# Performance work log

Measured on AMD Instinct MI355X. Metric: run time of the kernel, lower is better.

The kernel has to match this reference:

```python
import jax, jax.numpy as jnp
import numpy as np

# Config matching init_kwargs: num_heads=4, embedding_dim=1024 -> per-head dim 256,
# num_embeddings=8192. Defaults: hierarchical=False, transitions=False, gumbel=False,
# learnable_priors=False, relative_error=False, ema=True (so no q_latent_loss),
# use_straight_through=True, code_offset=0. Eval-mode path: hard argmin code selection.
H = 4
K = 8192
D = 1024
d = D // H
B = 8192
COMMITMENT_COST = 0.25
INIT_SCALE = 0.5


def setup_inputs() -> dict:
    key = jax.random.key(0)
    k1, k2 = jax.random.split(key)
    inputs = jax.random.normal(k1, (B, 1, D), dtype=jnp.float32)
    # embedding.weight.data.normal_(std=init_scale * init_decay_weight**hix), decay_weight=1.0
    codebooks = jax.random.normal(k2, (H, K, d), dtype=jnp.float32) * INIT_SCALE
    return {"inputs": inputs, "codebooks": codebooks}


def reference(inputs, codebooks):
    # inputs: [B, 1, D]; codebooks: [H, K, d]
    b = inputs.shape[0]
    x = inputs[:, 0, :].reshape(b, H, d)  # per-head slices of the latent

    x2 = jnp.sum(x * x, axis=-1)                       # [B, H]
    e2 = jnp.sum(codebooks * codebooks, axis=-1)       # [H, K]
    xe = jnp.einsum('bhd,hkd->bhk', x, codebooks)      # [B, H, K]
    dist = x2[..., None] - 2.0 * xe + e2[None, :, :]

    # Hard code selection (eval path: argmin over codebook)
    codes = jnp.argmin(dist, axis=-1)                  # [B, H] int

    # Gather quantized vectors: q[b, h] = codebooks[h, codes[b, h]]
    q = codebooks[jnp.arange(H)[None, :], codes]       # [B, H, d]

    # Commitment loss per sample (EMA mode => no codebook loss term):
    # F.mse_loss(quantized.detach(), this_input, reduction='none').mean(dim=-1), summed over heads
    e_latent = jnp.mean((jax.lax.stop_gradient(q) - x) ** 2, axis=-1)  # [B, H]
    loss = COMMITMENT_COST * jnp.sum(e_latent, axis=-1)                 # [B]

    # Straight-through estimator
    q_st = x + jax.lax.stop_gradient(q - x)            # [B, H, d]
    quantized = q_st.reshape(b, 1, D)

    return loss, quantized, codes
```

## Files before the change

kernel.cpp:

```cpp
#include <hip/hip_runtime.h>
#include <math.h>

#define HH 4
#define KK 8192
#define DD 1024
#define HD 256
#define BB 8192
#define MARGINF 1.0625f

typedef __attribute__((ext_vector_type(8))) short short8;
typedef __attribute__((ext_vector_type(4))) float floatx4;

__device__ __forceinline__ unsigned short f2bf(float f) {
    unsigned int u = __float_as_uint(f);
    u += 0x7FFFu + ((u >> 16) & 1u);
    return (unsigned short)(u >> 16);
}

__device__ __forceinline__ void gl_lds16(const unsigned short* g, char* l) {
    __builtin_amdgcn_global_load_lds(
        (const __attribute__((address_space(1))) unsigned int*)g,
        (__attribute__((address_space(3))) unsigned int*)l, 16, 0, 0);
}

__device__ __forceinline__ void gl_lds4(const float* g, char* l) {
    __builtin_amdgcn_global_load_lds(
        (const __attribute__((address_space(1))) unsigned int*)g,
        (__attribute__((address_space(3))) unsigned int*)l, 4, 0, 0);
}

__global__ __launch_bounds__(256)
void vq_e2(const float* __restrict__ C, float* __restrict__ e2w, float* __restrict__ e2p) {
    int gid  = blockIdx.x * 256 + threadIdx.x;
    int code = gid >> 2;
    int part = gid & 3;
    const float4* p = (const float4*)&C[(size_t)code * HD + part * 64];
    float s = 0.f;
#pragma unroll
    for (int i = 0; i < 16; ++i) {
        float4 v = p[i];
        s = fmaf(v.x, v.x, s); s = fmaf(v.y, v.y, s);
        s = fmaf(v.z, v.z, s); s = fmaf(v.w, v.w, s);
    }
    s += __shfl_xor(s, 1);
    s += __shfl_xor(s, 2);
    if (part == 0) { e2w[code] = s; e2p[code] = s + 1024.0f; }
}

__global__ __launch_bounds__(256)
void vq_cvtC(const float* __restrict__ C, unsigned short* __restrict__ Cbf) {
    size_t i = ((size_t)blockIdx.x * 256 + threadIdx.x) * 8;
    float4 a = *(const float4*)&C[i];
    float4 b = *(const float4*)&C[i + 4];
    short8 o;
    o[0] = (short)f2bf(a.x); o[1] = (short)f2bf(a.y); o[2] = (short)f2bf(a.z); o[3] = (short)f2bf(a.w);
    o[4] = (short)f2bf(b.x); o[5] = (short)f2bf(b.y); o[6] = (short)f2bf(b.z); o[7] = (short)f2bf(b.w);
    *(short8*)&Cbf[i] = o;
}

#define WAITV(N) asm volatile("s_waitcnt vmcnt(" #N ")" ::: "memory")
#define VQ_SYNC() do { __builtin_amdgcn_s_barrier(); __builtin_amdgcn_sched_barrier(0); } while (0)

#define VQ_STAGE(SB)                                                                                   \
    do {                                                                                               \
        const int ch1_ = (SB) >> 2, ks1_ = (SB) & 3;                                                   \
        _Pragma("unroll")                                                                              \
        for (int j = 0; j < 4; ++j) {                                                                  \
            const unsigned short* gp_ = CbfH + (size_t)(ch1_ * 128 + j * 32 + c0) * HD + ks1_ * 64 + ksegS * 8; \
            gl_lds16(gp_, smB + (((SB) & 3) << 14) + ((j * 256 + wid * 64) << 4));                     \
        }                                                                                              \
    } while (0)

#define VQ_STAGE_E2(CH2)                                                                               \
    do {                                                                                               \
        const int chc_ = (CH2) > 63 ? 63 : (CH2);                                                      \
        const float* gp_ = e2p + (size_t)h * KK + chc_ * 128 + ((wid & 1) << 6) + lane;                \
        gl_lds4(gp_, (char*)&e2ring[(((CH2) & 3) << 7) + ((wid & 1) << 6)]);                           \
    } while (0)

#define VQ_COMPUTE(KST, CH, S)                                                                         \
    do {                                                                                               \
        if ((KST) == 0) {                                                                              \
            e0 = e2ring[(((CH) & 3) << 7) + wid * 32 + cl];                                            \
            e1 = e2ring[(((CH) & 3) << 7) + wid * 32 + 16 + cl];                                       \
            floatx4 zz = {0.f, 0.f, 0.f, 0.f};                                                         \
            _Pragma("unroll")                                                                          \
            for (int tm = 0; tm < 4; ++tm) { acc[tm][0] = zz; acc[tm][1] = zz; }                       \
        }                                                                                              \
        const char* bb_ = smB + (((S) & 3) << 14);                                                     \
        __builtin_amdgcn_s_setprio(1);                                                                 \
        _Pragma("unroll")                                                                              \
        for (int kc = 0; kc < 2; ++kc) {                                                               \
            short8 b0 = *(const short8*)(bb_ + roff[0][kc]);                                           \
            short8 b1 = *(const short8*)(bb_ + roff[1][kc]);                                           \
            const int ai = (KST) * 2 + kc;                                                             \
            _Pragma("unroll")                                                                          \
            for (int tm = 0; tm < 4; ++tm) {                                                           \
                acc[tm][0] = __builtin_amdgcn_mfma_f32_16x16x32_bf16(afrag[tm][ai], b0, acc[tm][0], 0, 0, 0); \
                acc[tm][1] = __builtin_amdgcn_mfma_f32_16x16x32_bf16(afrag[tm][ai], b1, acc[tm][1], 0, 0, 0); \
            }                                                                                          \
        }                                                                                              \
        __builtin_amdgcn_s_setprio(0);                                                                 \
        if ((KST) == 3) {                                                                              \
            const int ctag = (CH) << 1;                                                                \
            _Pragma("unroll")                                                                          \
            for (int tn = 0; tn < 2; ++tn) {                                                           \
                const float ee = tn ? e1 : e0;                                                         \
                const int tag = ctag | tn;                                                             \
                _Pragma("unroll")                                                                      \
                for (int tm = 0; tm < 4; ++tm)                                                         \
                    _Pragma("unroll")                                                                  \
                    for (int r = 0; r < 4; ++r) {                                                      \
                        float dp = fmaf(-2.0f, acc[tm][tn][r], ee);                                    \
                        int key = (__float_as_int(dp) & 0xFFFFFF80) | tag;                             \
                        const int sl = tm * 4 + r;                                                     \
                        int mx = max(key, best1[sl]);                                                  \
                        best1[sl] = min(best1[sl], key);                                               \
                        best2[sl] = min(best2[sl], mx);                                                \
                    }                                                                                  \
            }                                                                                          \
        }                                                                                              \
    } while (0)

__global__ __launch_bounds__(256, 2)
void vq_score(const float* __restrict__ X, const float* __restrict__ C,
              const unsigned short* __restrict__ Cbf,
              const float* __restrict__ e2w, const float* __restrict__ e2p,
              float* __restrict__ elw,
              float* __restrict__ out_q, float* __restrict__ out_codes) {
    __shared__ __align__(16) char smB[65536];
    __shared__ float e2ring[512];
    __shared__ int   rowWave[256];
    __shared__ int   rowMinS[64];
    __shared__ int   cntA[64];
    __shared__ int   listI[64 * 8];
    __shared__ float pairD[128];
    __shared__ int   pairI[128];
    __shared__ int   codeS[64];

    const int tid = threadIdx.x;
    const int bi  = blockIdx.x;
    const int x   = bi & 7;
    const int h   = x & 3;
    const int rowbase = (((bi >> 3) << 1) + (x >> 2)) * 64;
    const int wid  = tid >> 6;
    const int lane = tid & 63;
    const int cl = lane & 15;
    const int qh = lane >> 4;

    short8 afrag[4][8];
#pragma unroll
    for (int tm = 0; tm < 4; ++tm) {
        const float* rp = X + (size_t)(rowbase + tm * 16 + cl) * DD + h * HD + qh * 8;
#pragma unroll
        for (int i = 0; i < 8; ++i) {
            float4 v0 = *(const float4*)(rp + i * 32);
            float4 v1 = *(const float4*)(rp + i * 32 + 4);
            short8 t;
            t[0] = (short)f2bf(v0.x); t[1] = (short)f2bf(v0.y); t[2] = (short)f2bf(v0.z); t[3] = (short)f2bf(v0.w);
            t[4] = (short)f2bf(v1.x); t[5] = (short)f2bf(v1.y); t[6] = (short)f2bf(v1.z); t[7] = (short)f2bf(v1.w);
            afrag[tm][i] = t;
        }
    }

    int best1[16], best2[16];
#pragma unroll
    for (int i = 0; i < 16; ++i) { best1[i] = 0x7FFFFFFF; best2[i] = 0x7FFFFFFF; }

    const unsigned short* CbfH = Cbf + (size_t)h * KK * HD;
    const int c0    = tid >> 3;
    const int ksegS = (tid & 7) ^ (c0 & 7);
    int roff[2][2];
#pragma unroll
    for (int tn = 0; tn < 2; ++tn)
#pragma unroll
        for (int kc = 0; kc < 2; ++kc)
            roff[tn][kc] = (wid * 32 + tn * 16 + cl) * 128 + ((((kc << 2) + qh) ^ (cl & 7)) << 4);

    floatx4 acc[4][2];
    float e0 = 0.f, e1 = 0.f;

    VQ_STAGE_E2(0);
    VQ_STAGE_E2(1);
    VQ_STAGE(0);
    VQ_STAGE(1);
    VQ_STAGE(2);

    for (int ch = 0; ch < 63; ++ch) {
        const int s0 = ch << 2;
        WAITV(8); VQ_SYNC(); VQ_STAGE(s0 + 3); VQ_STAGE_E2(ch + 2); VQ_COMPUTE(0, ch, s0 + 0);
        WAITV(9); VQ_SYNC(); VQ_STAGE(s0 + 4);                      VQ_COMPUTE(1, ch, s0 + 1);
        WAITV(9); VQ_SYNC(); VQ_STAGE(s0 + 5);                      VQ_COMPUTE(2, ch, s0 + 2);
        WAITV(9); VQ_SYNC(); VQ_STAGE(s0 + 6);                      VQ_COMPUTE(3, ch, s0 + 3);
    }
    WAITV(8); VQ_SYNC(); VQ_STAGE(255); VQ_COMPUTE(0, 63, 252);
    WAITV(8); VQ_SYNC();                VQ_COMPUTE(1, 63, 253);
    WAITV(4); VQ_SYNC();                VQ_COMPUTE(2, 63, 254);
    WAITV(0); VQ_SYNC();                VQ_COMPUTE(3, 63, 255);

#pragma unroll
    for (int sl = 0; sl < 16; ++sl) {
        int m = best1[sl];
        m = min(m, __shfl_xor(m, 1));
        m = min(m, __shfl_xor(m, 2));
        m = min(m, __shfl_xor(m, 4));
        m = min(m, __shfl_xor(m, 8));
        if (cl == 0) {
            int row = (sl >> 2) * 16 + qh * 4 + (sl & 3);
            rowWave[wid * 64 + row] = m;
        }
    }
    __syncthreads();
    if (tid < 64) {
        rowMinS[tid] = min(min(rowWave[tid], rowWave[64 + tid]),
                           min(rowWave[128 + tid], rowWave[192 + tid]));
        cntA[tid] = 0;
    }
    __syncthreads();
#pragma unroll
    for (int sl = 0; sl < 16; ++sl) {
        const int row = (sl >> 2) * 16 + qh * 4 + (sl & 3);
        const float lim = __int_as_float(rowMinS[row]) + MARGINF;
#pragma unroll
        for (int t = 0; t < 2; ++t) {
            int key = t ? best2[sl] : best1[sl];
            float d = __int_as_float(key & 0xFFFFFF80);
            if (d <= lim) {
                int chunk = (key >> 1) & 63, tn = key & 1;
                int code = chunk * 128 + wid * 32 + tn * 16 + cl;
                int pos = atomicAdd(&cntA[row], 1);
                if (pos < 8) listI[row * 8 + pos] = code;
            }
        }
    }
    __syncthreads();
    if (tid < 128) {
        int row = tid >> 1, par = tid & 1;
        int n = min(cntA[row], 8);
        float bD = 1e38f; int bI = 0x7FFFFFFF;
        if (n == 1) {
            if (par == 0) { bD = -1e38f; bI = listI[row * 8]; }
        } else {
            const float* Xr = X + (size_t)(rowbase + row) * DD + h * HD;
            float p0 = 0, p1 = 0, p2 = 0, p3 = 0;
            for (int d = 0;   d < 64;  ++d) p0 = fmaf(Xr[d], Xr[d], p0);
            for (int d = 64;  d < 128; ++d) p1 = fmaf(Xr[d], Xr[d], p1);
            for (int d = 128; d < 192; ++d) p2 = fmaf(Xr[d], Xr[d], p2);
            for (int d = 192; d < 256; ++d) p3 = fmaf(Xr[d], Xr[d], p3);
            float x2 = __fadd_rn(__fadd_rn(p0, p1), __fadd_rn(p2, p3));
            for (int j = par; j < n; j += 2) {
                int idx = listI[row * 8 + j];
                const float* Cr = C + ((size_t)h * KK + idx) * HD;
                float a = 0.f;
                for (int d = 0; d < 256; ++d) a = fmaf(Xr[d], Cr[d], a);
                float t1 = fmaf(-2.0f, a, x2);
                float dist = __fadd_rn(t1, e2w[h * KK + idx]);
                if (dist < bD || (dist == bD && idx < bI)) { bD = dist; bI = idx; }
            }
        }
        pairD[tid] = bD; pairI[tid] = bI;
    }
    __syncthreads();
    if (tid < 64) {
        float d0 = pairD[tid * 2], d1 = pairD[tid * 2 + 1];
        int   i0 = pairI[tid * 2], i1 = pairI[tid * 2 + 1];
        int w = (d1 < d0 || (d1 == d0 && i1 < i0)) ? i1 : i0;
        codeS[tid] = w;
        out_codes[(size_t)(rowbase + tid) * HH + h] = (float)w;
    }
    __syncthreads();

    {
        int row = tid >> 2, part = tid & 3;
        int b = rowbase + row;
        int c = codeS[row];
        const float4* qp = (const float4*)&C[((size_t)h * KK + c) * HD + part * 64];
        const float4* xp = (const float4*)&X[(size_t)b * DD + h * HD + part * 64];
        float4*       op = (float4*)&out_q[(size_t)b * DD + h * HD + part * 64];
        float s = 0.f;
#pragma unroll
        for (int i = 0; i < 16; ++i) {
            float4 q4 = qp[i]; float4 x4 = xp[i]; float4 o;
            float d0 = __fsub_rn(q4.x, x4.x); o.x = __fadd_rn(x4.x, d0); s = fmaf(d0, d0, s);
            float d1 = __fsub_rn(q4.y, x4.y); o.y = __fadd_rn(x4.y, d1); s = fmaf(d1, d1, s);
            float d2 = __fsub_rn(q4.z, x4.z); o.z = __fadd_rn(x4.z, d2); s = fmaf(d2, d2, s);
            float d3 = __fsub_rn(q4.w, x4.w); o.w = __fadd_rn(x4.w, d3); s = fmaf(d3, d3, s);
            op[i] = o;
        }
        s += __shfl_xor(s, 1);
        s += __shfl_xor(s, 2);
        if (part == 0) elw[(size_t)b * HH + h] = s * (1.0f / 256.0f);
    }
}

__global__ __launch_bounds__(256)
void vq_loss(const float* __restrict__ elw, float* __restrict__ out_loss) {
    int b = blockIdx.x * 256 + threadIdx.x;
    if (b < BB) {
        float4 e = *(const float4*)&elw[(size_t)b * HH];
        out_loss[b] = 0.25f * (((e.x + e.y) + e.z) + e.w);
    }
}

#define ROWS 64
#define KC   128
#define DC   32

__global__ __launch_bounds__(256, 3)
void vq_main(const float* __restrict__ X, const float* __restrict__ C,
             const float* __restrict__ e2w, float* __restrict__ elw,
             float* __restrict__ out_q, float* __restrict__ out_codes) {
    __shared__ float smem[2048 + 4096];
    float* Xs = smem;
    float* Cs = smem + 2048;
    __shared__ float x2s[ROWS];
    __shared__ int   codeSf[ROWS];

    const int tid     = threadIdx.x;
    const int h       = blockIdx.y;
    const int rowbase = blockIdx.x * ROWS;

    {
        int row = tid >> 2, part = tid & 3;
        const float4* xp = (const float4*)&X[(size_t)(rowbase + row) * DD + h * HD + part * 64];
        float s = 0.f;
#pragma unroll
        for (int i = 0; i < 16; ++i) {
            float4 v = xp[i];
            s = fmaf(v.x, v.x, s); s = fmaf(v.y, v.y, s);
            s = fmaf(v.z, v.z, s); s = fmaf(v.w, v.w, s);
        }
        s += __shfl_xor(s, 1);
        s += __shfl_xor(s, 2);
        if (part == 0) x2s[row] = s;
    }
    __syncthreads();

    const int rg = tid & 7;
    const int cg = tid >> 3;
    const int r0 = rg * 8;

    float x2r[8];
#pragma unroll
    for (int r = 0; r < 8; ++r) x2r[r] = x2s[r0 + r];

    float mn[8]; int mi[8];
#pragma unroll
    for (int r = 0; r < 8; ++r) { mn[r] = 3.402823466e38f; mi[r] = 0; }

    for (int kb = 0; kb < KK; kb += KC) {
        float acc[8][4];
#pragma unroll
        for (int r = 0; r < 8; ++r)
#pragma unroll
            for (int c = 0; c < 4; ++c) acc[r][c] = 0.f;

        for (int db = 0; db < HD; db += DC) {
            __syncthreads();
#pragma unroll
            for (int rep = 0; rep < 2; ++rep) {
                int i = tid + rep * 256;
                int row = i >> 3, q = i & 7;
                float4 v = *(const float4*)&X[(size_t)(rowbase + row) * DD + h * HD + db + q * 4];
                int col = row ^ ((q & 3) << 3);
                Xs[(q * 4 + 0) * 64 + col] = v.x;
                Xs[(q * 4 + 1) * 64 + col] = v.y;
                Xs[(q * 4 + 2) * 64 + col] = v.z;
                Xs[(q * 4 + 3) * 64 + col] = v.w;
            }
#pragma unroll
            for (int rep = 0; rep < 4; ++rep) {
                int i = tid + rep * 256;
                int code = i >> 3, q = i & 7;
                float4 v = *(const float4*)&C[((size_t)(h * KK + kb + code)) * HD + db + q * 4];
                int col = code ^ ((q & 3) << 3);
                Cs[(q * 4 + 0) * 128 + col] = v.x;
                Cs[(q * 4 + 1) * 128 + col] = v.y;
                Cs[(q * 4 + 2) * 128 + col] = v.z;
                Cs[(q * 4 + 3) * 128 + col] = v.w;
            }
            __syncthreads();
#pragma unroll
            for (int t = 0; t < DC; ++t) {
                int sw = ((t >> 2) & 3) << 3;
                const float4 xa = *(const float4*)&Xs[t * 64 + (r0 ^ sw)];
                const float4 xb = *(const float4*)&Xs[t * 64 + ((r0 ^ sw) + 4)];
                const float4 cv = *(const float4*)&Cs[t * 128 + ((cg * 4) ^ sw)];
                float xv[8] = {xa.x, xa.y, xa.z, xa.w, xb.x, xb.y, xb.z, xb.w};
                float clv[4] = {cv.x, cv.y, cv.z, cv.w};
#pragma unroll
                for (int r = 0; r < 8; ++r)
#pragma unroll
                    for (int c = 0; c < 4; ++c)
                        acc[r][c] = fmaf(xv[r], clv[c], acc[r][c]);
            }
        }
        const float4 e2v = *(const float4*)&e2w[h * KK + kb + cg * 4];
        float e2a[4] = {e2v.x, e2v.y, e2v.z, e2v.w};
#pragma unroll
        for (int c = 0; c < 4; ++c) {
            int kidx = kb + cg * 4 + c;
#pragma unroll
            for (int r = 0; r < 8; ++r) {
                float t1   = x2r[r] - 2.0f * acc[r][c];
                float dist = __fadd_rn(t1, e2a[c]);
                if (dist < mn[r]) { mn[r] = dist; mi[r] = kidx; }
            }
        }
    }

    __syncthreads();
    float* redm = smem;
    int*   redi = (int*)(smem + 2048);
#pragma unroll
    for (int r = 0; r < 8; ++r) {
        redm[cg * 64 + r0 + r] = mn[r];
        redi[cg * 64 + r0 + r] = mi[r];
    }
    __syncthreads();
    if (tid < ROWS) {
        int row = tid;
        float best = redm[row]; int bi2 = redi[row];
        for (int gg = 1; gg < 32; ++gg) {
            float m = redm[gg * 64 + row]; int ii = redi[gg * 64 + row];
            if (m < best || (m == best && ii < bi2)) { best = m; bi2 = ii; }
        }
        codeSf[row] = bi2;
        out_codes[(size_t)(rowbase + row) * HH + h] = (float)bi2;
    }
    __syncthreads();

    {
        int row = tid >> 2, part = tid & 3;
        int b = rowbase + row;
        int c = codeSf[row];
        const float4* qp = (const float4*)&C[((size_t)(h * KK + c)) * HD + part * 64];
        const float4* xp = (const float4*)&X[(size_t)b * DD + h * HD + part * 64];
        float4*       op = (float4*)&out_q[(size_t)b * DD + h * HD + part * 64];
        float s = 0.f;
#pragma unroll
        for (int i = 0; i < 16; ++i) {
            float4 q4 = qp[i]; float4 x4 = xp[i]; float4 o;
            float d0 = __fsub_rn(q4.x, x4.x); o.x = __fadd_rn(x4.x, d0); s = fmaf(d0, d0, s);
            float d1 = __fsub_rn(q4.y, x4.y); o.y = __fadd_rn(x4.y, d1); s = fmaf(d1, d1, s);
            float d2 = __fsub_rn(q4.z, x4.z); o.z = __fadd_rn(x4.z, d2); s = fmaf(d2, d2, s);
            float d3 = __fsub_rn(q4.w, x4.w); o.w = __fadd_rn(x4.w, d3); s = fmaf(d3, d3, s);
            op[i] = o;
        }
        s += __shfl_xor(s, 1);
        s += __shfl_xor(s, 2);
        if (part == 0) elw[(size_t)b * HH + h] = s * (1.0f / 256.0f);
    }
}

extern "C" void kernel_launch(void* const* d_in, const int* in_sizes, int n_in,
                              void* d_out, int out_size, void* d_ws, size_t ws_size,
                              hipStream_t stream) {
    const float* X = (const float*)d_in[0];
    const float* C = (const float*)d_in[1];
    float* out      = (float*)d_out;
    float* out_loss = out;
    float* out_q    = out + BB;
    float* out_code = out + BB + (size_t)BB * DD;
    float* e2w = (float*)d_ws;
    float* e2p = e2w + (size_t)HH * KK;
    float* elw = e2p + (size_t)HH * KK;
    unsigned short* Cbf = (unsigned short*)(elw + (size_t)BB * HH);

    const size_t need = ((size_t)2 * HH * KK + (size_t)BB * HH) * 4 + (size_t)HH * KK * HD * 2;

    if (ws_size >= need) {
        vq_e2<<<512, 256, 0, stream>>>(C, e2w, e2p);
        vq_cvtC<<<(HH * KK * HD / 8) / 256, 256, 0, stream>>>(C, Cbf);
        vq_score<<<512, 256, 0, stream>>>(X, C, Cbf, e2w, e2p, elw, out_q, out_code);
        vq_loss<<<BB / 256, 256, 0, stream>>>(elw, out_loss);
    } else {
        vq_e2<<<512, 256, 0, stream>>>(C, e2w, e2p);
        dim3 grid(BB / ROWS, HH);
        vq_main<<<grid, 256, 0, stream>>>(X, C, e2w, elw, out_q, out_code);
        vq_loss<<<BB / 256, 256, 0, stream>>>(elw, out_loss);
    }
}
```

Before: 306.1 us.

## Double score-block rows to 128 with 512 threads and fuse codebook prep kernels

```diff
diff --git a/kernel.cpp b/kernel.cpp
--- a/kernel.cpp
+++ b/kernel.cpp
@@ -27,6 +27,33 @@
     __builtin_amdgcn_global_load_lds(
         (const __attribute__((address_space(1))) unsigned int*)g,
         (__attribute__((address_space(3))) unsigned int*)l, 4, 0, 0);
+}
+
+__global__ __launch_bounds__(256)
+void vq_prep(const float* __restrict__ C, unsigned short* __restrict__ Cbf,
+             float* __restrict__ e2w, float* __restrict__ e2p) {
+    int gid  = blockIdx.x * 256 + threadIdx.x;
+    int code = gid >> 2;
+    int part = gid & 3;
+    const float4* p = (const float4*)&C[(size_t)code * HD + part * 64];
+    short8* ob = (short8*)&Cbf[(size_t)code * HD + part * 64];
+    float s = 0.f;
+#pragma unroll
+    for (int i = 0; i < 8; ++i) {
+        float4 a = p[2 * i];
+        float4 b = p[2 * i + 1];
+        s = fmaf(a.x, a.x, s); s = fmaf(a.y, a.y, s);
+        s = fmaf(a.z, a.z, s); s = fmaf(a.w, a.w, s);
+        s = fmaf(b.x, b.x, s); s = fmaf(b.y, b.y, s);
+        s = fmaf(b.z, b.z, s); s = fmaf(b.w, b.w, s);
+        short8 o;
+        o[0] = (short)f2bf(a.x); o[1] = (short)f2bf(a.y); o[2] = (short)f2bf(a.z); o[3] = (short)f2bf(a.w);
+        o[4] = (short)f2bf(b.x); o[5] = (short)f2bf(b.y); o[6] = (short)f2bf(b.z); o[7] = (short)f2bf(b.w);
+        ob[i] = o;
+    }
+    s += __shfl_xor(s, 1);
+    s += __shfl_xor(s, 2);
+    if (part == 0) { e2w[code] = s; e2p[code] = s + 1024.0f; }
 }
 
 __global__ __launch_bounds__(256)
@@ -47,53 +74,42 @@
     if (part == 0) { e2w[code] = s; e2p[code] = s + 1024.0f; }
 }
 
-__global__ __launch_bounds__(256)
-void vq_cvtC(const float* __restrict__ C, unsigned short* __restrict__ Cbf) {
-    size_t i = ((size_t)blockIdx.x * 256 + threadIdx.x) * 8;
-    float4 a = *(const float4*)&C[i];
-    float4 b = *(const float4*)&C[i + 4];
-    short8 o;
-    o[0] = (short)f2bf(a.x); o[1] = (short)f2bf(a.y); o[2] = (short)f2bf(a.z); o[3] = (short)f2bf(a.w);
-    o[4] = (short)f2bf(b.x); o[5] = (short)f2bf(b.y); o[6] = (short)f2bf(b.z); o[7] = (short)f2bf(b.w);
-    *(short8*)&Cbf[i] = o;
-}
-
 #define WAITV(N) asm volatile("s_waitcnt vmcnt(" #N ")" ::: "memory")
 #define VQ_SYNC() do { __builtin_amdgcn_s_barrier(); __builtin_amdgcn_sched_barrier(0); } while (0)
 
 #define VQ_STAGE(SB)                                                                                   \
     do {                                                                                               \
-        const int ch1_ = (SB) >> 2, ks1_ = (SB) & 3;                                                   \
+        const int ch_ = (SB) >> 1, kh_ = (SB) & 1;                                                     \
         _Pragma("unroll")                                                                              \
         for (int j = 0; j < 4; ++j) {                                                                  \
-            const unsigned short* gp_ = CbfH + (size_t)(ch1_ * 128 + j * 32 + c0) * HD + ks1_ * 64 + ksegS * 8; \
-            gl_lds16(gp_, smB + (((SB) & 3) << 14) + ((j * 256 + wid * 64) << 4));                     \
+            const unsigned short* gp_ = CbfH + (size_t)(ch_ * 128 + j * 32 + (tid >> 4)) * HD          \
+                                        + kh_ * 128 + ksegS * 8;                                       \
+            gl_lds16(gp_, smB + (((SB) & 3) << 15) + ((j * 512 + wid * 64) << 4));                     \
         }                                                                                              \
     } while (0)
 
 #define VQ_STAGE_E2(CH2)                                                                               \
     do {                                                                                               \
-        const int chc_ = (CH2) > 63 ? 63 : (CH2);                                                      \
-        const float* gp_ = e2p + (size_t)h * KK + chc_ * 128 + ((wid & 1) << 6) + lane;                \
+        const float* gp_ = e2p + (size_t)h * KK + (CH2) * 128 + ((wid & 1) << 6) + lane;               \
         gl_lds4(gp_, (char*)&e2ring[(((CH2) & 3) << 7) + ((wid & 1) << 6)]);                           \
     } while (0)
 
 #define VQ_COMPUTE(KST, CH, S)                                                                         \
     do {                                                                                               \
         if ((KST) == 0) {                                                                              \
-            e0 = e2ring[(((CH) & 3) << 7) + wid * 32 + cl];                                            \
-            e1 = e2ring[(((CH) & 3) << 7) + wid * 32 + 16 + cl];                                       \
+            e0 = e2ring[(((CH) & 3) << 7) + wq * 32 + cl];                                             \
+            e1 = e2ring[(((CH) & 3) << 7) + wq * 32 + 16 + cl];                                        \
             floatx4 zz = {0.f, 0.f, 0.f, 0.f};                                                         \
             _Pragma("unroll")                                                                          \
             for (int tm = 0; tm < 4; ++tm) { acc[tm][0] = zz; acc[tm][1] = zz; }                       \
         }                                                                                              \
-        const char* bb_ = smB + (((S) & 3) << 14);                                                     \
+        const char* bb_ = smB + (((S) & 3) << 15);                                                     \
         __builtin_amdgcn_s_setprio(1);                                                                 \
         _Pragma("unroll")                                                                              \
-        for (int kc = 0; kc < 2; ++kc) {                                                               \
-            short8 b0 = *(const short8*)(bb_ + roff[0][kc]);                                           \
-            short8 b1 = *(const short8*)(bb_ + roff[1][kc]);                                           \
-            const int ai = (KST) * 2 + kc;                                                             \
+        for (int ks = 0; ks < 4; ++ks) {                                                               \
+            short8 b0 = *(const short8*)(bb_ + roff[0][ks]);                                           \
+            short8 b1 = *(const short8*)(bb_ + roff[1][ks]);                                           \
+            const int ai = (KST) * 4 + ks;                                                             \
             _Pragma("unroll")                                                                          \
             for (int tm = 0; tm < 4; ++tm) {                                                           \
                 acc[tm][0] = __builtin_amdgcn_mfma_f32_16x16x32_bf16(afrag[tm][ai], b0, acc[tm][0], 0, 0, 0); \
@@ -101,7 +117,7 @@
             }                                                                                          \
         }                                                                                              \
         __builtin_amdgcn_s_setprio(0);                                                                 \
-        if ((KST) == 3) {                                                                              \
+        if ((KST) == 1) {                                                                              \
             const int ctag = (CH) << 1;                                                                \
             _Pragma("unroll")                                                                          \
             for (int tn = 0; tn < 2; ++tn) {                                                           \
@@ -114,44 +130,46 @@
                         float dp = fmaf(-2.0f, acc[tm][tn][r], ee);                                    \
                         int key = (__float_as_int(dp) & 0xFFFFFF80) | tag;                             \
                         const int sl = tm * 4 + r;                                                     \
-                        int mx = max(key, best1[sl]);                                                  \
-                        best1[sl] = min(best1[sl], key);                                               \
-                        best2[sl] = min(best2[sl], mx);                                                \
+                        int b1o = best1[sl];                                                           \
+                        best1[sl] = min(b1o, key);                                                     \
+                        best2[sl] = min(best2[sl], max(key, b1o));                   \
                     }                                                                                  \
             }                                                                                          \
         }                                                                                              \
     } while (0)
 
-__global__ __launch_bounds__(256, 2)
+__global__ __launch_bounds__(512, 2)
 void vq_score(const float* __restrict__ X, const float* __restrict__ C,
               const unsigned short* __restrict__ Cbf,
               const float* __restrict__ e2w, const float* __restrict__ e2p,
               float* __restrict__ elw,
               float* __restrict__ out_q, float* __restrict__ out_codes) {
-    __shared__ __align__(16) char smB[65536];
+    __shared__ __align__(16) char smB[131072];
     __shared__ float e2ring[512];
-    __shared__ int   rowWave[256];
-    __shared__ int   rowMinS[64];
-    __shared__ int   cntA[64];
-    __shared__ int   listI[64 * 8];
-    __shared__ float pairD[128];
-    __shared__ int   pairI[128];
-    __shared__ int   codeS[64];
+    __shared__ int   rowWave[512];
+    __shared__ int   rowMinS[128];
+    __shared__ int   cntA[128];
+    __shared__ int   listI[128 * 8];
+    __shared__ float pairD[256];
+    __shared__ int   pairI[256];
+    __shared__ int   codeS[128];
 
     const int tid = threadIdx.x;
     const int bi  = blockIdx.x;
     const int x   = bi & 7;
     const int h   = x & 3;
-    const int rowbase = (((bi >> 3) << 1) + (x >> 2)) * 64;
+    const int rowbase = (((bi >> 3) << 1) + (x >> 2)) * 128;
     const int wid  = tid >> 6;
     const int lane = tid & 63;
     const int cl = lane & 15;
     const int qh = lane >> 4;
+    const int wq = wid & 3;
+    const int rh = wid >> 2;
 
     short8 afrag[4][8];
 #pragma unroll
     for (int tm = 0; tm < 4; ++tm) {
-        const float* rp = X + (size_t)(rowbase + tm * 16 + cl) * DD + h * HD + qh * 8;
+        const float* rp = X + (size_t)(rowbase + rh * 64 + tm * 16 + cl) * DD + h * HD + qh * 8;
 #pragma unroll
         for (int i = 0; i < 8; ++i) {
             float4 v0 = *(const float4*)(rp + i * 32);
@@ -168,35 +186,34 @@
     for (int i = 0; i < 16; ++i) { best1[i] = 0x7FFFFFFF; best2[i] = 0x7FFFFFFF; }
 
     const unsigned short* CbfH = Cbf + (size_t)h * KK * HD;
-    const int c0    = tid >> 3;
-    const int ksegS = (tid & 7) ^ (c0 & 7);
-    int roff[2][2];
+    const int ksegS = (tid & 15) ^ ((tid >> 4) & 15);
+    int roff[2][4];
 #pragma unroll
     for (int tn = 0; tn < 2; ++tn)
 #pragma unroll
-        for (int kc = 0; kc < 2; ++kc)
-            roff[tn][kc] = (wid * 32 + tn * 16 + cl) * 128 + ((((kc << 2) + qh) ^ (cl & 7)) << 4);
+        for (int ks = 0; ks < 4; ++ks)
+            roff[tn][ks] = (wq * 32 + tn * 16 + cl) * 256 + ((((ks << 2) + qh) ^ cl) << 4);
 
     floatx4 acc[4][2];
     float e0 = 0.f, e1 = 0.f;
 
+    asm volatile("s_waitcnt vmcnt(0)" ::: "memory");
+
     VQ_STAGE_E2(0);
+    VQ_STAGE(0);
     VQ_STAGE_E2(1);
-    VQ_STAGE(0);
     VQ_STAGE(1);
     VQ_STAGE(2);
 
-    for (int ch = 0; ch < 63; ++ch) {
-        const int s0 = ch << 2;
-        WAITV(8); VQ_SYNC(); VQ_STAGE(s0 + 3); VQ_STAGE_E2(ch + 2); VQ_COMPUTE(0, ch, s0 + 0);
+    for (int ch = 0; ch < 62; ++ch) {
+        const int s0 = ch << 1;
+        WAITV(9); VQ_SYNC(); VQ_STAGE(s0 + 3); VQ_STAGE_E2(ch + 2); VQ_COMPUTE(0, ch, s0);
         WAITV(9); VQ_SYNC(); VQ_STAGE(s0 + 4);                      VQ_COMPUTE(1, ch, s0 + 1);
-        WAITV(9); VQ_SYNC(); VQ_STAGE(s0 + 5);                      VQ_COMPUTE(2, ch, s0 + 2);
-        WAITV(9); VQ_SYNC(); VQ_STAGE(s0 + 6);                      VQ_COMPUTE(3, ch, s0 + 3);
-    }
-    WAITV(8); VQ_SYNC(); VQ_STAGE(255); VQ_COMPUTE(0, 63, 252);
-    WAITV(8); VQ_SYNC();                VQ_COMPUTE(1, 63, 253);
-    WAITV(4); VQ_SYNC();                VQ_COMPUTE(2, 63, 254);
-    WAITV(0); VQ_SYNC();                VQ_COMPUTE(3, 63, 255);
+    }
+    WAITV(9); VQ_SYNC(); VQ_STAGE(127); VQ_COMPUTE(0, 62, 124);
+    WAITV(9); VQ_SYNC();                VQ_COMPUTE(1, 62, 125);
+    WAITV(4); VQ_SYNC();                VQ_COMPUTE(0, 63, 126);
+    WAITV(0); VQ_SYNC();                VQ_COMPUTE(1, 63, 127);
 
 #pragma unroll
     for (int sl = 0; sl < 16; ++sl) {
@@ -206,20 +223,20 @@
         m = min(m, __shfl_xor(m, 4));
         m = min(m, __shfl_xor(m, 8));
         if (cl == 0) {
-            int row = (sl >> 2) * 16 + qh * 4 + (sl & 3);
-            rowWave[wid * 64 + row] = m;
-        }
-    }
-    __syncthreads();
-    if (tid < 64) {
-        rowMinS[tid] = min(min(rowWave[tid], rowWave[64 + tid]),
-                           min(rowWave[128 + tid], rowWave[192 + tid]));
+            int row = rh * 64 + (sl >> 2) * 16 + qh * 4 + (sl & 3);
+            rowWave[wq * 128 + row] = m;
+        }
+    }
+    __syncthreads();
+    if (tid < 128) {
+        rowMinS[tid] = min(min(rowWave[tid], rowWave[128 + tid]),
+                           min(rowWave[256 + tid], rowWave[384 + tid]));
         cntA[tid] = 0;
     }
     __syncthreads();
 #pragma unroll
     for (int sl = 0; sl < 16; ++sl) {
-        const int row = (sl >> 2) * 16 + qh * 4 + (sl & 3);
+        const int row = rh * 64 + (sl >> 2) * 16 + qh * 4 + (sl & 3);
         const float lim = __int_as_float(rowMinS[row]) + MARGINF;
 #pragma unroll
         for (int t = 0; t < 2; ++t) {
@@ -227,14 +244,14 @@
             float d = __int_as_float(key & 0xFFFFFF80);
             if (d <= lim) {
                 int chunk = (key >> 1) & 63, tn = key & 1;
-                int code = chunk * 128 + wid * 32 + tn * 16 + cl;
+                int code = chunk * 128 + wq * 32 + tn * 16 + cl;
                 int pos = atomicAdd(&cntA[row], 1);
                 if (pos < 8) listI[row * 8 + pos] = code;
             }
         }
     }
     __syncthreads();
-    if (tid < 128) {
+    if (tid < 256) {
         int row = tid >> 1, par = tid & 1;
         int n = min(cntA[row], 8);
         float bD = 1e38f; int bI = 0x7FFFFFFF;
@@ -261,7 +278,7 @@
         pairD[tid] = bD; pairI[tid] = bI;
     }
     __syncthreads();
-    if (tid < 64) {
+    if (tid < 128) {
         float d0 = pairD[tid * 2], d1 = pairD[tid * 2 + 1];
         int   i0 = pairI[tid * 2], i1 = pairI[tid * 2 + 1];
         int w = (d1 < d0 || (d1 == d0 && i1 < i0)) ? i1 : i0;
@@ -470,9 +487,8 @@
     const size_t need = ((size_t)2 * HH * KK + (size_t)BB * HH) * 4 + (size_t)HH * KK * HD * 2;
 
     if (ws_size >= need) {
-        vq_e2<<<512, 256, 0, stream>>>(C, e2w, e2p);
-        vq_cvtC<<<(HH * KK * HD / 8) / 256, 256, 0, stream>>>(C, Cbf);
-        vq_score<<<512, 256, 0, stream>>>(X, C, Cbf, e2w, e2p, elw, out_q, out_code);
+        vq_prep<<<512, 256, 0, stream>>>(C, Cbf, e2w, e2p);
+        vq_score<<<256, 512, 0, stream>>>(X, C, Cbf, e2w, e2p, elw, out_q, out_code);
         vq_loss<<<BB / 256, 256, 0, stream>>>(elw, out_loss);
     } else {
         vq_e2<<<512, 256, 0, stream>>>(C, e2w, e2p);
```

Measured after the change: 318.8 us. +4.1%, slower.

## Fuse prep kernels, drop block barriers via per-wave staging, fold loss into score

Applied to the files above, without the earlier changes.

```diff
diff --git a/kernel.cpp b/kernel.cpp
--- a/kernel.cpp
+++ b/kernel.cpp
@@ -11,6 +11,8 @@
 typedef __attribute__((ext_vector_type(8))) short short8;
 typedef __attribute__((ext_vector_type(4))) float floatx4;
 
+__device__ unsigned int vq_cnt[128];
+
 __device__ __forceinline__ unsigned short f2bf(float f) {
     unsigned int u = __float_as_uint(f);
     u += 0x7FFFu + ((u >> 16) & 1u);
@@ -27,6 +29,33 @@
     __builtin_amdgcn_global_load_lds(
         (const __attribute__((address_space(1))) unsigned int*)g,
         (__attribute__((address_space(3))) unsigned int*)l, 4, 0, 0);
+}
+
+__global__ __launch_bounds__(256)
+void vq_prep(const float* __restrict__ C, unsigned short* __restrict__ Cbf,
+             float* __restrict__ e2w, float* __restrict__ e2p) {
+    int gid  = blockIdx.x * 256 + threadIdx.x;
+    int code = gid >> 2;
+    int part = gid & 3;
+    const float4* p = (const float4*)&C[(size_t)code * HD + part * 64];
+    short8* ob = (short8*)&Cbf[(size_t)code * HD + part * 64];
+    float s = 0.f;
+#pragma unroll
+    for (int i = 0; i < 8; ++i) {
+        float4 a = p[2 * i];
+        float4 b = p[2 * i + 1];
+        s = fmaf(a.x, a.x, s); s = fmaf(a.y, a.y, s);
+        s = fmaf(a.z, a.z, s); s = fmaf(a.w, a.w, s);
+        s = fmaf(b.x, b.x, s); s = fmaf(b.y, b.y, s);
+        s = fmaf(b.z, b.z, s); s = fmaf(b.w, b.w, s);
+        short8 o;
+        o[0] = (short)f2bf(a.x); o[1] = (short)f2bf(a.y); o[2] = (short)f2bf(a.z); o[3] = (short)f2bf(a.w);
+        o[4] = (short)f2bf(b.x); o[5] = (short)f2bf(b.y); o[6] = (short)f2bf(b.z); o[7] = (short)f2bf(b.w);
+        ob[i] = o;
+    }
+    s += __shfl_xor(s, 1);
+    s += __shfl_xor(s, 2);
+    if (part == 0) { e2w[code] = s; e2p[code] = s + 1024.0f; }
 }
 
 __global__ __launch_bounds__(256)
@@ -47,42 +76,35 @@
     if (part == 0) { e2w[code] = s; e2p[code] = s + 1024.0f; }
 }
 
-__global__ __launch_bounds__(256)
-void vq_cvtC(const float* __restrict__ C, unsigned short* __restrict__ Cbf) {
-    size_t i = ((size_t)blockIdx.x * 256 + threadIdx.x) * 8;
-    float4 a = *(const float4*)&C[i];
-    float4 b = *(const float4*)&C[i + 4];
-    short8 o;
-    o[0] = (short)f2bf(a.x); o[1] = (short)f2bf(a.y); o[2] = (short)f2bf(a.z); o[3] = (short)f2bf(a.w);
-    o[4] = (short)f2bf(b.x); o[5] = (short)f2bf(b.y); o[6] = (short)f2bf(b.z); o[7] = (short)f2bf(b.w);
-    *(short8*)&Cbf[i] = o;
-}
-
-#define WAITV(N) asm volatile("s_waitcnt vmcnt(" #N ")" ::: "memory")
-#define VQ_SYNC() do { __builtin_amdgcn_s_barrier(); __builtin_amdgcn_sched_barrier(0); } while (0)
+#define WAITV(N)                                                                                       \
+    do {                                                                                               \
+        asm volatile("s_waitcnt vmcnt(" #N ")" ::: "memory");                                          \
+        __builtin_amdgcn_sched_barrier(0);                                                             \
+    } while (0)
 
 #define VQ_STAGE(SB)                                                                                   \
     do {                                                                                               \
-        const int ch1_ = (SB) >> 2, ks1_ = (SB) & 3;                                                   \
+        const int ch_ = (SB) >> 2, ks_ = (SB) & 3;                                                     \
         _Pragma("unroll")                                                                              \
         for (int j = 0; j < 4; ++j) {                                                                  \
-            const unsigned short* gp_ = CbfH + (size_t)(ch1_ * 128 + j * 32 + c0) * HD + ks1_ * 64 + ksegS * 8; \
-            gl_lds16(gp_, smB + (((SB) & 3) << 14) + ((j * 256 + wid * 64) << 4));                     \
+            const unsigned short* gp_ = CbfH + (size_t)(ch_ * 128 + wid * 32 + j * 8 + (lane >> 3)) * HD \
+                                        + ks_ * 64 + kseg2 * 8;                                        \
+            gl_lds16(gp_, smB + (((SB) & 3) << 14) + (wid << 12) + (j << 10));                         \
         }                                                                                              \
     } while (0)
 
 #define VQ_STAGE_E2(CH2)                                                                               \
     do {                                                                                               \
         const int chc_ = (CH2) > 63 ? 63 : (CH2);                                                      \
-        const float* gp_ = e2p + (size_t)h * KK + chc_ * 128 + ((wid & 1) << 6) + lane;                \
-        gl_lds4(gp_, (char*)&e2ring[(((CH2) & 3) << 7) + ((wid & 1) << 6)]);                           \
+        const float* gp_ = e2p + (size_t)h * KK + chc_ * 128 + wid * 32 + (lane & 31);                 \
+        gl_lds4(gp_, (char*)e2ring + (wid << 10) + (((CH2) & 3) << 8));                                \
     } while (0)
 
 #define VQ_COMPUTE(KST, CH, S)                                                                         \
     do {                                                                                               \
         if ((KST) == 0) {                                                                              \
-            e0 = e2ring[(((CH) & 3) << 7) + wid * 32 + cl];                                            \
-            e1 = e2ring[(((CH) & 3) << 7) + wid * 32 + 16 + cl];                                       \
+            e0 = e2ring[wid * 256 + (((CH) & 3) << 6) + cl];                                           \
+            e1 = e2ring[wid * 256 + (((CH) & 3) << 6) + 16 + cl];                                      \
             floatx4 zz = {0.f, 0.f, 0.f, 0.f};                                                         \
             _Pragma("unroll")                                                                          \
             for (int tm = 0; tm < 4; ++tm) { acc[tm][0] = zz; acc[tm][1] = zz; }                       \
@@ -114,9 +136,9 @@
                         float dp = fmaf(-2.0f, acc[tm][tn][r], ee);                                    \
                         int key = (__float_as_int(dp) & 0xFFFFFF80) | tag;                             \
                         const int sl = tm * 4 + r;                                                     \
-                        int mx = max(key, best1[sl]);                                                  \
-                        best1[sl] = min(best1[sl], key);                                               \
-                        best2[sl] = min(best2[sl], mx);                                                \
+                        int b1o = best1[sl];                                                           \
+                        best1[sl] = min(b1o, key);                                                     \
+                        best2[sl] = min(best2[sl], max(key, b1o));                                     \
                     }                                                                                  \
             }                                                                                          \
         }                                                                                              \
@@ -127,9 +149,10 @@
               const unsigned short* __restrict__ Cbf,
               const float* __restrict__ e2w, const float* __restrict__ e2p,
               float* __restrict__ elw,
-              float* __restrict__ out_q, float* __restrict__ out_codes) {
+              float* __restrict__ out_q, float* __restrict__ out_codes,
+              float* __restrict__ out_loss) {
     __shared__ __align__(16) char smB[65536];
-    __shared__ float e2ring[512];
+    __shared__ float e2ring[1024];
     __shared__ int   rowWave[256];
     __shared__ int   rowMinS[64];
     __shared__ int   cntA[64];
@@ -137,6 +160,7 @@
     __shared__ float pairD[128];
     __shared__ int   pairI[128];
     __shared__ int   codeS[64];
+    __shared__ int   lastFlag;
 
     const int tid = threadIdx.x;
     const int bi  = blockIdx.x;
@@ -168,8 +192,7 @@
     for (int i = 0; i < 16; ++i) { best1[i] = 0x7FFFFFFF; best2[i] = 0x7FFFFFFF; }
 
     const unsigned short* CbfH = Cbf + (size_t)h * KK * HD;
-    const int c0    = tid >> 3;
-    const int ksegS = (tid & 7) ^ (c0 & 7);
+    const int kseg2 = (lane & 7) ^ ((lane >> 3) & 7);
     int roff[2][2];
 #pragma unroll
     for (int tn = 0; tn < 2; ++tn)
@@ -180,23 +203,25 @@
     floatx4 acc[4][2];
     float e0 = 0.f, e1 = 0.f;
 
+    asm volatile("s_waitcnt vmcnt(0)" ::: "memory");
+
     VQ_STAGE_E2(0);
+    VQ_STAGE(0);
     VQ_STAGE_E2(1);
-    VQ_STAGE(0);
     VQ_STAGE(1);
     VQ_STAGE(2);
 
     for (int ch = 0; ch < 63; ++ch) {
         const int s0 = ch << 2;
-        WAITV(8); VQ_SYNC(); VQ_STAGE(s0 + 3); VQ_STAGE_E2(ch + 2); VQ_COMPUTE(0, ch, s0 + 0);
-        WAITV(9); VQ_SYNC(); VQ_STAGE(s0 + 4);                      VQ_COMPUTE(1, ch, s0 + 1);
-        WAITV(9); VQ_SYNC(); VQ_STAGE(s0 + 5);                      VQ_COMPUTE(2, ch, s0 + 2);
-        WAITV(9); VQ_SYNC(); VQ_STAGE(s0 + 6);                      VQ_COMPUTE(3, ch, s0 + 3);
-    }
-    WAITV(8); VQ_SYNC(); VQ_STAGE(255); VQ_COMPUTE(0, 63, 252);
-    WAITV(8); VQ_SYNC();                VQ_COMPUTE(1, 63, 253);
-    WAITV(4); VQ_SYNC();                VQ_COMPUTE(2, 63, 254);
-    WAITV(0); VQ_SYNC();                VQ_COMPUTE(3, 63, 255);
+        WAITV(8); VQ_STAGE(s0 + 3); VQ_STAGE_E2(ch + 2); VQ_COMPUTE(0, ch, s0);
+        WAITV(9); VQ_STAGE(s0 + 4);                      VQ_COMPUTE(1, ch, s0 + 1);
+        WAITV(9); VQ_STAGE(s0 + 5);                      VQ_COMPUTE(2, ch, s0 + 2);
+        WAITV(9); VQ_STAGE(s0 + 6);                      VQ_COMPUTE(3, ch, s0 + 3);
+    }
+    WAITV(8); VQ_STAGE(255); VQ_COMPUTE(0, 63, 252);
+    WAITV(8);                VQ_COMPUTE(1, 63, 253);
+    WAITV(4);                VQ_COMPUTE(2, 63, 254);
+    WAITV(0);                VQ_COMPUTE(3, 63, 255);
 
 #pragma unroll
     for (int sl = 0; sl < 16; ++sl) {
@@ -289,7 +314,26 @@
         }
         s += __shfl_xor(s, 1);
         s += __shfl_xor(s, 2);
-        if (part == 0) elw[(size_t)b * HH + h] = s * (1.0f / 256.0f);
+        if (part == 0) elw[(size_t)h * BB + b] = s * (1.0f / 256.0f);
+    }
+
+    __threadfence();
+    __syncthreads();
+    if (tid == 0) {
+        unsigned int old = atomicAdd(&vq_cnt[rowbase >> 6], 1u);
+        lastFlag = ((old & 3u) == 3u) ? 1 : 0;
+    }
+    __syncthreads();
+    if (lastFlag) {
+        __threadfence();
+        if (tid < 64) {
+            int b = rowbase + tid;
+            float ev0 = elw[0 * BB + b];
+            float ev1 = elw[1 * BB + b];
+            float ev2 = elw[2 * BB + b];
+            float ev3 = elw[3 * BB + b];
+            out_loss[b] = 0.25f * (((ev0 + ev1) + ev2) + ev3);
+        }
     }
 }
 
@@ -470,10 +514,8 @@
     const size_t need = ((size_t)2 * HH * KK + (size_t)BB * HH) * 4 + (size_t)HH * KK * HD * 2;
 
     if (ws_size >= need) {
-        vq_e2<<<512, 256, 0, stream>>>(C, e2w, e2p);
-        vq_cvtC<<<(HH * KK * HD / 8) / 256, 256, 0, stream>>>(C, Cbf);
-        vq_score<<<512, 256, 0, stream>>>(X, C, Cbf, e2w, e2p, elw, out_q, out_code);
-        vq_loss<<<BB / 256, 256, 0, stream>>>(elw, out_loss);
+        vq_prep<<<512, 256, 0, stream>>>(C, Cbf, e2w, e2p);
+        vq_score<<<512, 256, 0, stream>>>(X, C, Cbf, e2w, e2p, elw, out_q, out_code, out_loss);
     } else {
         vq_e2<<<512, 256, 0, stream>>>(C, e2w, e2p);
         dim3 grid(BB / ROWS, HH);
```

Result: slower. 440.5 us (+43.9%).

## Deepen LDS staging ring to eight stages and fuse codebook prep kernels

Applied to the files above, without the earlier changes.

```diff
diff --git a/kernel.cpp b/kernel.cpp
--- a/kernel.cpp
+++ b/kernel.cpp
@@ -27,6 +27,33 @@
     __builtin_amdgcn_global_load_lds(
         (const __attribute__((address_space(1))) unsigned int*)g,
         (__attribute__((address_space(3))) unsigned int*)l, 4, 0, 0);
+}
+
+__global__ __launch_bounds__(256)
+void vq_prep(const float* __restrict__ C, unsigned short* __restrict__ Cbf,
+             float* __restrict__ e2w, float* __restrict__ e2p) {
+    int gid  = blockIdx.x * 256 + threadIdx.x;
+    int code = gid >> 2;
+    int part = gid & 3;
+    const float4* p = (const float4*)&C[(size_t)code * HD + part * 64];
+    short8* ob = (short8*)&Cbf[(size_t)code * HD + part * 64];
+    float s = 0.f;
+#pragma unroll
+    for (int i = 0; i < 8; ++i) {
+        float4 a = p[2 * i];
+        float4 b = p[2 * i + 1];
+        s = fmaf(a.x, a.x, s); s = fmaf(a.y, a.y, s);
+        s = fmaf(a.z, a.z, s); s = fmaf(a.w, a.w, s);
+        s = fmaf(b.x, b.x, s); s = fmaf(b.y, b.y, s);
+        s = fmaf(b.z, b.z, s); s = fmaf(b.w, b.w, s);
+        short8 o;
+        o[0] = (short)f2bf(a.x); o[1] = (short)f2bf(a.y); o[2] = (short)f2bf(a.z); o[3] = (short)f2bf(a.w);
+        o[4] = (short)f2bf(b.x); o[5] = (short)f2bf(b.y); o[6] = (short)f2bf(b.z); o[7] = (short)f2bf(b.w);
+        ob[i] = o;
+    }
+    s += __shfl_xor(s, 1);
+    s += __shfl_xor(s, 2);
+    if (part == 0) { e2w[code] = s; e2p[code] = s + 1024.0f; }
 }
 
 __global__ __launch_bounds__(256)
@@ -47,34 +74,22 @@
     if (part == 0) { e2w[code] = s; e2p[code] = s + 1024.0f; }
 }
 
-__global__ __launch_bounds__(256)
-void vq_cvtC(const float* __restrict__ C, unsigned short* __restrict__ Cbf) {
-    size_t i = ((size_t)blockIdx.x * 256 + threadIdx.x) * 8;
-    float4 a = *(const float4*)&C[i];
-    float4 b = *(const float4*)&C[i + 4];
-    short8 o;
-    o[0] = (short)f2bf(a.x); o[1] = (short)f2bf(a.y); o[2] = (short)f2bf(a.z); o[3] = (short)f2bf(a.w);
-    o[4] = (short)f2bf(b.x); o[5] = (short)f2bf(b.y); o[6] = (short)f2bf(b.z); o[7] = (short)f2bf(b.w);
-    *(short8*)&Cbf[i] = o;
-}
-
 #define WAITV(N) asm volatile("s_waitcnt vmcnt(" #N ")" ::: "memory")
 #define VQ_SYNC() do { __builtin_amdgcn_s_barrier(); __builtin_amdgcn_sched_barrier(0); } while (0)
 
 #define VQ_STAGE(SB)                                                                                   \
     do {                                                                                               \
-        const int ch1_ = (SB) >> 2, ks1_ = (SB) & 3;                                                   \
+        const int ch_ = (SB) >> 2, ks_ = (SB) & 3;                                                     \
         _Pragma("unroll")                                                                              \
         for (int j = 0; j < 4; ++j) {                                                                  \
-            const unsigned short* gp_ = CbfH + (size_t)(ch1_ * 128 + j * 32 + c0) * HD + ks1_ * 64 + ksegS * 8; \
-            gl_lds16(gp_, smB + (((SB) & 3) << 14) + ((j * 256 + wid * 64) << 4));                     \
+            const unsigned short* gp_ = CbfH + (size_t)(ch_ * 128 + j * 32 + c0) * HD + ks_ * 64 + ksegS * 8; \
+            gl_lds16(gp_, smB + (((SB) & 7) << 14) + ((j * 256 + wid * 64) << 4));                     \
         }                                                                                              \
     } while (0)
 
 #define VQ_STAGE_E2(CH2)                                                                               \
     do {                                                                                               \
-        const int chc_ = (CH2) > 63 ? 63 : (CH2);                                                      \
-        const float* gp_ = e2p + (size_t)h * KK + chc_ * 128 + ((wid & 1) << 6) + lane;                \
+        const float* gp_ = e2p + (size_t)h * KK + (CH2) * 128 + ((wid & 1) << 6) + lane;               \
         gl_lds4(gp_, (char*)&e2ring[(((CH2) & 3) << 7) + ((wid & 1) << 6)]);                           \
     } while (0)
 
@@ -87,7 +102,7 @@
             _Pragma("unroll")                                                                          \
             for (int tm = 0; tm < 4; ++tm) { acc[tm][0] = zz; acc[tm][1] = zz; }                       \
         }                                                                                              \
-        const char* bb_ = smB + (((S) & 3) << 14);                                                     \
+        const char* bb_ = smB + (((S) & 7) << 14);                                                     \
         __builtin_amdgcn_s_setprio(1);                                                                 \
         _Pragma("unroll")                                                                              \
         for (int kc = 0; kc < 2; ++kc) {                                                               \
@@ -114,9 +129,9 @@
                         float dp = fmaf(-2.0f, acc[tm][tn][r], ee);                                    \
                         int key = (__float_as_int(dp) & 0xFFFFFF80) | tag;                             \
                         const int sl = tm * 4 + r;                                                     \
-                        int mx = max(key, best1[sl]);                                                  \
-                        best1[sl] = min(best1[sl], key);                                               \
-                        best2[sl] = min(best2[sl], mx);                                                \
+                        int b1o = best1[sl];                                                           \
+                        best1[sl] = min(b1o, key);                                                     \
+                        best2[sl] = min(best2[sl], max(key, b1o));                                     \
                     }                                                                                  \
             }                                                                                          \
         }                                                                                              \
@@ -128,7 +143,7 @@
               const float* __restrict__ e2w, const float* __restrict__ e2p,
               float* __restrict__ elw,
               float* __restrict__ out_q, float* __restrict__ out_codes) {
-    __shared__ __align__(16) char smB[65536];
+    __shared__ __align__(16) char smB[131072];
     __shared__ float e2ring[512];
     __shared__ int   rowWave[256];
     __shared__ int   rowMinS[64];
@@ -180,23 +195,38 @@
     floatx4 acc[4][2];
     float e0 = 0.f, e1 = 0.f;
 
+    asm volatile("s_waitcnt vmcnt(0)" ::: "memory");
+
     VQ_STAGE_E2(0);
     VQ_STAGE_E2(1);
     VQ_STAGE(0);
     VQ_STAGE(1);
     VQ_STAGE(2);
-
-    for (int ch = 0; ch < 63; ++ch) {
+    VQ_STAGE(3);
+    VQ_STAGE(4);
+    VQ_STAGE(5);
+    VQ_STAGE(6);
+
+    WAITV(24); VQ_SYNC(); VQ_STAGE(7);  VQ_STAGE_E2(2); VQ_COMPUTE(0, 0, 0);
+    WAITV(25); VQ_SYNC(); VQ_STAGE(8);                  VQ_COMPUTE(1, 0, 1);
+    WAITV(25); VQ_SYNC(); VQ_STAGE(9);                  VQ_COMPUTE(2, 0, 2);
+    WAITV(25); VQ_SYNC(); VQ_STAGE(10);                 VQ_COMPUTE(3, 0, 3);
+
+    for (int ch = 1; ch < 62; ++ch) {
         const int s0 = ch << 2;
-        WAITV(8); VQ_SYNC(); VQ_STAGE(s0 + 3); VQ_STAGE_E2(ch + 2); VQ_COMPUTE(0, ch, s0 + 0);
-        WAITV(9); VQ_SYNC(); VQ_STAGE(s0 + 4);                      VQ_COMPUTE(1, ch, s0 + 1);
-        WAITV(9); VQ_SYNC(); VQ_STAGE(s0 + 5);                      VQ_COMPUTE(2, ch, s0 + 2);
-        WAITV(9); VQ_SYNC(); VQ_STAGE(s0 + 6);                      VQ_COMPUTE(3, ch, s0 + 3);
-    }
-    WAITV(8); VQ_SYNC(); VQ_STAGE(255); VQ_COMPUTE(0, 63, 252);
-    WAITV(8); VQ_SYNC();                VQ_COMPUTE(1, 63, 253);
-    WAITV(4); VQ_SYNC();                VQ_COMPUTE(2, 63, 254);
-    WAITV(0); VQ_SYNC();                VQ_COMPUTE(3, 63, 255);
+        WAITV(25); VQ_SYNC(); VQ_STAGE(s0 + 7);  VQ_STAGE_E2(ch + 2); VQ_COMPUTE(0, ch, s0);
+        WAITV(26); VQ_SYNC(); VQ_STAGE(s0 + 8);                       VQ_COMPUTE(1, ch, s0 + 1);
+        WAITV(26); VQ_SYNC(); VQ_STAGE(s0 + 9);                       VQ_COMPUTE(2, ch, s0 + 2);
+        WAITV(26); VQ_SYNC(); VQ_STAGE(s0 + 10);                      VQ_COMPUTE(3, ch, s0 + 3);
+    }
+    WAITV(25); VQ_SYNC(); VQ_STAGE(255); VQ_COMPUTE(0, 62, 248);
+    WAITV(25); VQ_SYNC();                VQ_COMPUTE(1, 62, 249);
+    WAITV(21); VQ_SYNC();                VQ_COMPUTE(2, 62, 250);
+    WAITV(17); VQ_SYNC();                VQ_COMPUTE(3, 62, 251);
+    WAITV(12); VQ_SYNC(); VQ_COMPUTE(0, 63, 252);
+    WAITV(8);  VQ_SYNC(); VQ_COMPUTE(1, 63, 253);
+    WAITV(4);  VQ_SYNC(); VQ_COMPUTE(2, 63, 254);
+    WAITV(0);  VQ_SYNC(); VQ_COMPUTE(3, 63, 255);
 
 #pragma unroll
     for (int sl = 0; sl < 16; ++sl) {
@@ -470,8 +500,7 @@
     const size_t need = ((size_t)2 * HH * KK + (size_t)BB * HH) * 4 + (size_t)HH * KK * HD * 2;
 
     if (ws_size >= need) {
-        vq_e2<<<512, 256, 0, stream>>>(C, e2w, e2p);
-        vq_cvtC<<<(HH * KK * HD / 8) / 256, 256, 0, stream>>>(C, Cbf);
+        vq_prep<<<512, 256, 0, stream>>>(C, Cbf, e2w, e2p);
         vq_score<<<512, 256, 0, stream>>>(X, C, Cbf, e2w, e2p, elw, out_q, out_code);
         vq_loss<<<BB / 256, 256, 0, stream>>>(elw, out_loss);
     } else {
```

Result: slower. 390.0 us (+27.4%).
